# Optimization experiments

Hardware: AMD Instinct MI355X
Metric: run time of the kernel (lower is better)

The kernel has to match this reference:

```python
import jax, jax.numpy as jnp
import numpy as np

IN_DIM = 64
OUT_DIM = 64
ATTN_DIM = 5
N_REL = 200
N_ENT = 40000
N_NODE = 500000
N_EDGE = 1000000
BATCH = 32


def setup_inputs() -> dict:
    key = jax.random.key(0)
    ks = jax.random.split(key, 20)
    n_rel_emb = 2 * N_REL + 1
    # forward args
    q_sub = jax.random.randint(ks[0], (BATCH,), 0, N_ENT)
    q_rel = jax.random.randint(ks[1], (BATCH,), 0, n_rel_emb)
    hidden = jax.random.normal(ks[2], (N_NODE, IN_DIM), dtype=jnp.float32)
    # edges columns: 0=batch idx, 1=unused, 2=rel, 3=unused, 4=sub, 5=obj
    e_batch = jax.random.randint(ks[3], (N_EDGE,), 0, BATCH)
    e_rel = jax.random.randint(ks[4], (N_EDGE,), 0, n_rel_emb)
    e_sub = jax.random.randint(ks[5], (N_EDGE,), 0, N_NODE)
    e_obj = jax.random.randint(ks[6], (N_EDGE,), 0, N_NODE)
    edges = jnp.stack([e_batch, e_batch, e_rel, e_rel, e_sub, e_obj], axis=1)
    nodes = jnp.stack([jax.random.randint(ks[7], (N_NODE,), 0, BATCH),
                       jax.random.randint(ks[8], (N_NODE,), 0, N_ENT)], axis=1)
    old_nodes_new_idx = jax.random.randint(ks[9], (100000,), 0, N_NODE)
    # parameters (stored as [in, out]; torch Linear does x @ W.T + b)
    def lin(k, fan_in, fan_out):
        b = 1.0 / np.sqrt(fan_in)
        return jax.random.uniform(k, (fan_in, fan_out), jnp.float32, -b, b)
    rela_embed = jax.random.normal(ks[10], (n_rel_emb, IN_DIM), dtype=jnp.float32)
    return {
        "hidden": hidden,
        "rela_embed": rela_embed,
        "Ws": lin(ks[11], IN_DIM, ATTN_DIM),
        "Wr": lin(ks[12], IN_DIM, ATTN_DIM),
        "Wqr_w": lin(ks[13], IN_DIM, ATTN_DIM),
        "Wqr_b": jnp.zeros((ATTN_DIM,), jnp.float32),
        "walpha_w": lin(ks[14], ATTN_DIM, 1),
        "walpha_b": jnp.zeros((1,), jnp.float32),
        "Wh": lin(ks[15], IN_DIM, OUT_DIM),
        "attn_fc_w": lin(ks[16], 2 * OUT_DIM, 1),
        "attn_fc_b": jnp.zeros((1,), jnp.float32),
        "Wnode_w": lin(ks[17], OUT_DIM, OUT_DIM),
        "Wnode_b": jnp.zeros((OUT_DIM,), jnp.float32),
        "q_sub": q_sub,
        "q_rel": q_rel,
        "edges": edges,
        "nodes": nodes,
        "old_nodes_new_idx": old_nodes_new_idx,
        "batchsize": BATCH,
    }


def reference(hidden, rela_embed, Ws, Wr, Wqr_w, Wqr_b, walpha_w, walpha_b,
              Wh, attn_fc_w, attn_fc_b, Wnode_w, Wnode_b,
              q_sub, q_rel, edges, nodes, old_nodes_new_idx, batchsize):
    n_node = nodes.shape[0]
    r_idx, rel, sub, obj = edges[:, 0], edges[:, 2], edges[:, 4], edges[:, 5]
    hs = hidden[sub]                      # [E, in_dim] gather
    hr = rela_embed[rel]                  # [E, in_dim]
    h_qr = rela_embed[q_rel][r_idx]       # [E, in_dim]
    message = hs - hr                     # [E, in_dim]
    attn = jax.nn.relu(hs @ Ws + hr @ Wr + h_qr @ Wqr_w + Wqr_b)   # [E, attn_dim]
    alpha = jax.nn.sigmoid(attn @ walpha_w + walpha_b)             # [E, 1]
    message = alpha * message
    # scatter-max over obj; empty segments filled with 0 (torch_scatter semantics)
    agg = jax.ops.segment_max(message, obj, num_segments=n_node)   # [n_node, in_dim]
    agg = jnp.where(jnp.isneginf(agg), 0.0, agg)
    hidden_new = agg @ Wh                 # act = identity        [n_node, out_dim]
    # edge attention over new node states
    cat = jnp.concatenate([hidden_new[sub], hidden_new[obj]], axis=-1)  # [E, 2*out]
    scores = jax.nn.leaky_relu((cat @ attn_fc_w + attn_fc_b)[:, 0], 0.2)  # [E]
    # source code overwrites scatter_softmax with a global softmax over all edges
    w = jax.nn.softmax(scores)            # [E]
    msg2 = w[:, None] * (hidden_new[obj] @ Wnode_w + Wnode_b)      # [E, out_dim]
    hidden_new = jax.ops.segment_sum(msg2, sub, num_segments=n_node)
    return hidden_new
```

## Files before the change

### kernel.cpp

```cpp
#include <hip/hip_runtime.h>
#include <math.h>
#include <float.h>


#define SCAN_BLK 256
#define SCAN_ITEMS 4
#define SCAN_CHUNK (SCAN_BLK * SCAN_ITEMS)
#define SOFT_G 2048
#define NPW 8

__global__ void k_tables(const float* __restrict__ rela, const float* __restrict__ Wr,
                         const float* __restrict__ Wqr_w, const float* __restrict__ Wqr_b,
                         const int* __restrict__ q_rel,
                         float* __restrict__ s2, float* __restrict__ s3,
                         int nrel, int batch) {
  int tid = blockIdx.x * blockDim.x + threadIdx.x;
  int stride = gridDim.x * blockDim.x;
  for (int idx = tid; idx < nrel * 5; idx += stride) {
    int r = idx / 5, j = idx % 5;
    float acc = 0.f;
    for (int k = 0; k < 64; k++) acc += rela[r * 64 + k] * Wr[k * 5 + j];
    s2[idx] = acc;
  }
  for (int idx = tid; idx < batch * 5; idx += stride) {
    int b = idx / 5, j = idx % 5;
    int qr = q_rel[b];
    float acc = Wqr_b[j];
    for (int k = 0; k < 64; k++) acc += rela[qr * 64 + k] * Wqr_w[k * 5 + j];
    s3[idx] = acc;
  }
}

__global__ void k_fuse(const float* __restrict__ Wh, const float* __restrict__ Wn,
                       const float* __restrict__ fw,
                       float* __restrict__ W2, float* __restrict__ fuv) {
  int tid = threadIdx.x;
  for (int idx = tid; idx < 64 * 64; idx += 256) {
    int k = idx >> 6, m = idx & 63;
    float acc = 0.f;
    for (int j = 0; j < 64; j++) acc += Wh[k * 64 + j] * Wn[j * 64 + m];
    W2[idx] = acc;
  }
  if (tid < 128) {
    int k = tid & 63, h = tid >> 6;
    float acc = 0.f;
    for (int j = 0; j < 64; j++) acc += Wh[k * 64 + j] * fw[h * 64 + j];
    fuv[h * 64 + k] = acc;
  }
}

__global__ void __launch_bounds__(256, 2)
k_proj(const float* __restrict__ hidden, const float* __restrict__ Ws_g,
       float* __restrict__ P, int N) {
  int n = blockIdx.x * blockDim.x + threadIdx.x;
  if (n >= N) return;
  float hs[64];
  const float4* h4 = (const float4*)(hidden + (size_t)n * 64);
#pragma unroll
  for (int k4 = 0; k4 < 16; k4++) {
    float4 h = h4[k4];
    hs[k4 * 4 + 0] = h.x; hs[k4 * 4 + 1] = h.y; hs[k4 * 4 + 2] = h.z; hs[k4 * 4 + 3] = h.w;
  }
  float acc[5] = {0.f, 0.f, 0.f, 0.f, 0.f};
#pragma unroll
  for (int k = 0; k < 64; k++) {
    float h = hs[k];
#pragma unroll
    for (int j = 0; j < 5; j++) acc[j] += h * Ws_g[k * 5 + j];
  }
#pragma unroll
  for (int j = 0; j < 5; j++) P[(size_t)n * 5 + j] = acc[j];
}

__global__ void k_hist(const int* __restrict__ edges, int* __restrict__ cnt, int E, int N) {
  int e = blockIdx.x * blockDim.x + threadIdx.x;
  if (e < E) {
    int sub = edges[e * 6 + 4];
    int obj = edges[e * 6 + 5];
    atomicAdd(&cnt[obj], 1);
    atomicAdd(&cnt[N + sub], 1);
  }
}

__global__ void k_scan_partial(const int* __restrict__ cnt, int* __restrict__ part, int n) {
  __shared__ int sdata[SCAN_BLK];
  int base = blockIdx.x * SCAN_CHUNK + threadIdx.x * SCAN_ITEMS;
  int s = 0;
#pragma unroll
  for (int j = 0; j < SCAN_ITEMS; j++) { int i = base + j; if (i < n) s += cnt[i]; }
  sdata[threadIdx.x] = s;
  __syncthreads();
  for (int d = SCAN_BLK / 2; d > 0; d >>= 1) {
    if (threadIdx.x < d) sdata[threadIdx.x] += sdata[threadIdx.x + d];
    __syncthreads();
  }
  if (threadIdx.x == 0) part[blockIdx.x] = sdata[0];
}

__global__ void k_scan_top(int* part, int nblk) {
  __shared__ int lds[1024];
  int tid = threadIdx.x;
  int v = (tid < nblk) ? part[tid] : 0;
  lds[tid] = v;
  __syncthreads();
  for (int d = 1; d < 1024; d <<= 1) {
    int t = (tid >= d) ? lds[tid - d] : 0;
    __syncthreads();
    lds[tid] += t;
    __syncthreads();
  }
  if (tid < nblk) part[tid] = lds[tid] - v;
}

__global__ void k_scan_final(const int* __restrict__ cnt, const int* __restrict__ part,
                             int* __restrict__ off, int n) {
  __shared__ int lds[SCAN_BLK];
  int tid = threadIdx.x;
  int base = blockIdx.x * SCAN_CHUNK + tid * SCAN_ITEMS;
  int c[SCAN_ITEMS];
  int s = 0;
#pragma unroll
  for (int j = 0; j < SCAN_ITEMS; j++) { int i = base + j; c[j] = (i < n) ? cnt[i] : 0; s += c[j]; }
  int v = s;
  lds[tid] = s;
  __syncthreads();
  for (int d = 1; d < SCAN_BLK; d <<= 1) {
    int t = (tid >= d) ? lds[tid - d] : 0;
    __syncthreads();
    lds[tid] += t;
    __syncthreads();
  }
  int run = part[blockIdx.x] + (lds[tid] - v);
#pragma unroll
  for (int j = 0; j < SCAN_ITEMS; j++) { int i = base + j; if (i < n) off[i] = run; run += c[j]; }
}

__global__ void k_scatter(const int* __restrict__ edges, const float* __restrict__ P,
                          const float* __restrict__ s2, const float* __restrict__ s3,
                          const float* __restrict__ walpha_w, const float* __restrict__ walpha_b,
                          int* __restrict__ cur, int4* __restrict__ rec_obj,
                          int2* __restrict__ rec_sub, int E, int N) {
  int e = blockIdx.x * blockDim.x + threadIdx.x;
  if (e >= E) return;
  int ridx = edges[e * 6 + 0];
  int rel  = edges[e * 6 + 2];
  int sub  = edges[e * 6 + 4];
  int obj  = edges[e * 6 + 5];
  float z = walpha_b[0];
#pragma unroll
  for (int j = 0; j < 5; j++) {
    float vj = P[(size_t)sub * 5 + j] + s2[rel * 5 + j] + s3[ridx * 5 + j];
    z += fmaxf(vj, 0.f) * walpha_w[j];
  }
  float a = 1.f / (1.f + expf(-z));
  int p = atomicAdd(&cur[obj], 1);
  rec_obj[p] = make_int4(sub, rel, __float_as_int(a), 0);
  int q = atomicAdd(&cur[N + sub], 1) - E;
  rec_sub[q] = make_int2(obj, sub);
}

__global__ void k_agg(const int* __restrict__ off, const int4* __restrict__ rec_obj,
                      const float* __restrict__ hidden, const float* __restrict__ rela,
                      float* __restrict__ agg, int N) {
  int lane = threadIdx.x & 63;
  int wid  = blockIdx.x * (blockDim.x >> 6) + (threadIdx.x >> 6);
  int node0 = wid * NPW;
  if (node0 >= N) return;
  int ov = 0;
  if (lane <= NPW) {
    int idx = node0 + lane;
    if (idx > N) idx = N;
    ov = off[idx];
  }
  int B   = __shfl(ov, 0);
  int End = __shfl(ov, NPW);
  int lbase = B;
  int rx = 0, ry = 0; float rz = 0.f;
  {
    int p = lbase + lane;
    if (p < End) { int4 r = rec_obj[p]; rx = r.x; ry = r.y; rz = __int_as_float(r.z); }
  }
  int cur = B;
  for (int i = 0; i < NPW; i++) {
    int node = node0 + i;
    if (node >= N) break;
    int en = __shfl(ov, i + 1);
    int bst = cur;
    float vmax = -FLT_MAX;
    while (cur < en) {
      int idx = cur - lbase;
      if (idx >= 64) {
        lbase += 64;
        int p = lbase + lane;
        if (p < End) { int4 r = rec_obj[p]; rx = r.x; ry = r.y; rz = __int_as_float(r.z); }
        idx = 0;
      }
      int sub = __shfl(rx, idx);
      int rel = __shfl(ry, idx);
      float a = __shfl(rz, idx);
      float x = a * (hidden[(size_t)sub * 64 + lane] - rela[rel * 64 + lane]);
      vmax = fmaxf(vmax, x);
      cur++;
    }
    agg[(size_t)node * 64 + lane] = (en > bst) ? vmax : 0.f;
  }
}

__global__ void __launch_bounds__(128)
k_trans(float* A, const float* __restrict__ W2, const float* __restrict__ fuv,
        float* __restrict__ u, float* __restrict__ v, int N) {
  __shared__ float lds[64 * 64];
  int tid = threadIdx.x;
  int n0 = blockIdx.x * 128;
  int n = n0 + tid;
  bool act = (n < N);
  float acc[64];
  if (act) {
    float a[64];
    const float4* A4 = (const float4*)(A + (size_t)n * 64);
#pragma unroll
    for (int q = 0; q < 16; q++) {
      float4 h = A4[q];
      a[q * 4 + 0] = h.x; a[q * 4 + 1] = h.y; a[q * 4 + 2] = h.z; a[q * 4 + 3] = h.w;
    }
    float uacc = 0.f, vacc = 0.f;
#pragma unroll
    for (int k = 0; k < 64; k++) {
      uacc += a[k] * fuv[k];
      vacc += a[k] * fuv[64 + k];
    }
    u[n] = uacc;
    v[n] = vacc;
#pragma unroll
    for (int j = 0; j < 64; j++) acc[j] = 0.f;
#pragma unroll
    for (int k = 0; k < 64; k++) {
      float ak = a[k];
#pragma unroll
      for (int j = 0; j < 64; j++) acc[j] += ak * W2[k * 64 + j];
    }
  }
  for (int ph = 0; ph < 2; ph++) {
    if (act && (tid >> 6) == ph) {
      int r = tid & 63;
#pragma unroll
      for (int g = 0; g < 16; g++) {
        int pos = g ^ (tid & 15);
        *(float4*)&lds[r * 64 + pos * 4] =
            make_float4(acc[g * 4], acc[g * 4 + 1], acc[g * 4 + 2], acc[g * 4 + 3]);
      }
    }
    __syncthreads();
    float4* Cg = (float4*)(A + (size_t)(n0 + ph * 64) * 64);
#pragma unroll
    for (int i = 0; i < 8; i++) {
      int f = tid + 128 * i;
      int row = f >> 4, c4 = f & 15;
      if (n0 + ph * 64 + row < N) {
        int pos = c4 ^ (row & 15);
        Cg[f] = *(float4*)&lds[row * 64 + pos * 4];
      }
    }
    __syncthreads();
  }
}

__global__ void k_scores(const int2* __restrict__ rec_sub, const float* __restrict__ u,
                         const float* __restrict__ v, const float* __restrict__ fb,
                         float* __restrict__ scores, float* __restrict__ pmax,
                         float* __restrict__ psum, int E) {
  __shared__ float red_m[256], red_s[256];
  float b = fb[0];
  float lm = -FLT_MAX, ls = 0.f;
  for (int pos = blockIdx.x * blockDim.x + threadIdx.x; pos < E; pos += gridDim.x * blockDim.x) {
    int2 r = rec_sub[pos];
    float s = u[r.y] + v[r.x] + b;
    s = (s >= 0.f) ? s : 0.2f * s;
    scores[pos] = s;
    if (s > lm) { ls = ls * expf(lm - s) + 1.f; lm = s; }
    else        { ls += expf(s - lm); }
  }
  red_m[threadIdx.x] = lm; red_s[threadIdx.x] = ls;
  __syncthreads();
  for (int d = blockDim.x / 2; d > 0; d >>= 1) {
    if (threadIdx.x < d) {
      float m1 = red_m[threadIdx.x], s1 = red_s[threadIdx.x];
      float m2 = red_m[threadIdx.x + d], s2 = red_s[threadIdx.x + d];
      float m = fmaxf(m1, m2);
      float s = 0.f;
      if (m > -FLT_MAX) s = s1 * expf(m1 - m) + s2 * expf(m2 - m);
      red_m[threadIdx.x] = m; red_s[threadIdx.x] = s;
    }
    __syncthreads();
  }
  if (threadIdx.x == 0) { pmax[blockIdx.x] = red_m[0]; psum[blockIdx.x] = red_s[0]; }
}

__global__ void k_softmax_final(const float* __restrict__ pmax, const float* __restrict__ psum,
                                float* __restrict__ scal, int G) {
  __shared__ float red_m[256], red_s[256];
  float lm = -FLT_MAX, ls = 0.f;
  for (int i = threadIdx.x; i < G; i += 256) {
    float m2 = pmax[i], s2 = psum[i];
    if (m2 > lm) { ls = ls * expf(lm - m2) + s2; lm = m2; }
    else         { ls += s2 * expf(m2 - lm); }
  }
  red_m[threadIdx.x] = lm; red_s[threadIdx.x] = ls;
  __syncthreads();
  for (int d = 128; d > 0; d >>= 1) {
    if (threadIdx.x < d) {
      float m1 = red_m[threadIdx.x], s1 = red_s[threadIdx.x];
      float m2 = red_m[threadIdx.x + d], s2 = red_s[threadIdx.x + d];
      float m = fmaxf(m1, m2);
      float s = 0.f;
      if (m > -FLT_MAX) s = s1 * expf(m1 - m) + s2 * expf(m2 - m);
      red_m[threadIdx.x] = m; red_s[threadIdx.x] = s;
    }
    __syncthreads();
  }
  if (threadIdx.x == 0) { scal[0] = red_m[0]; scal[1] = red_s[0]; }
}

__global__ void k_expw(float* __restrict__ scores, const float* __restrict__ scal, int E) {
  int i = blockIdx.x * blockDim.x + threadIdx.x;
  if (i < E) scores[i] = expf(scores[i] - scal[0]);
}

__global__ void k_aggsum(const int* __restrict__ off, const int2* __restrict__ rec_sub,
                         const float* __restrict__ wexp, const float* __restrict__ agg2,
                         const float* __restrict__ bias, const float* __restrict__ scal,
                         float* __restrict__ out, int N, int E) {
  int lane = threadIdx.x & 63;
  int wid  = blockIdx.x * (blockDim.x >> 6) + (threadIdx.x >> 6);
  int node0 = wid * NPW;
  if (node0 >= N) return;
  float bl = bias[lane];
  float inv = 1.f / scal[1];
  int ov = 0;
  if (lane <= NPW) {
    int idx = node0 + lane;
    ov = (idx >= N) ? E : (off[N + idx] - E);
  }
  int B   = __shfl(ov, 0);
  int End = __shfl(ov, NPW);
  int lbase = B;
  int objr = 0; float wr = 0.f;
  {
    int p = lbase + lane;
    if (p < End) { objr = rec_sub[p].x; wr = wexp[p]; }
  }
  int cur = B;
  for (int i = 0; i < NPW; i++) {
    int node = node0 + i;
    if (node >= N) break;
    int en = __shfl(ov, i + 1);
    float acc = 0.f, wa = 0.f;
    while (cur < en) {
      int idx = cur - lbase;
      if (idx >= 64) {
        lbase += 64;
        int p = lbase + lane;
        if (p < End) { objr = rec_sub[p].x; wr = wexp[p]; }
        idx = 0;
      }
      int obj = __shfl(objr, idx);
      float ww = __shfl(wr, idx);
      acc += ww * agg2[(size_t)obj * 64 + lane];
      wa  += ww;
      cur++;
    }
    out[(size_t)node * 64 + lane] = (acc + wa * bl) * inv;
  }
}

extern "C" void kernel_launch(void* const* d_in, const int* in_sizes, int n_in,
                              void* d_out, int out_size, void* d_ws, size_t ws_size,
                              hipStream_t stream) {
  const float* hidden    = (const float*)d_in[0];
  const float* rela      = (const float*)d_in[1];
  const float* Ws        = (const float*)d_in[2];
  const float* Wr        = (const float*)d_in[3];
  const float* Wqr_w     = (const float*)d_in[4];
  const float* Wqr_b     = (const float*)d_in[5];
  const float* walpha_w  = (const float*)d_in[6];
  const float* walpha_b  = (const float*)d_in[7];
  const float* Wh        = (const float*)d_in[8];
  const float* attn_fc_w = (const float*)d_in[9];
  const float* attn_fc_b = (const float*)d_in[10];
  const float* Wnode_w   = (const float*)d_in[11];
  const float* Wnode_b   = (const float*)d_in[12];
  const int*   q_rel     = (const int*)d_in[14];
  const int*   edges     = (const int*)d_in[15];

  int N = in_sizes[0] / 64;
  int E = in_sizes[15] / 6;
  int nrel = in_sizes[1] / 64;
  int batch = in_sizes[14];

  char* w = (char*)d_ws;
  size_t o = 0;
  #define WS_ALLOC(ptr_t, name, bytes) \
    ptr_t name = (ptr_t)(w + o); o = (o + (size_t)(bytes) + 255) & ~(size_t)255;
  WS_ALLOC(float*, aggT,    (size_t)N * 64 * 4)
  WS_ALLOC(float*, P,       (size_t)N * 5 * 4)
  WS_ALLOC(int4*,  rec_obj, (size_t)E * 16)
  WS_ALLOC(int2*,  rec_sub, (size_t)E * 8)
  WS_ALLOC(int*,   cnt,     (size_t)2 * N * 4)
  WS_ALLOC(int*,   off,     (size_t)2 * N * 4)
  WS_ALLOC(int*,   part,    1024 * 4)
  WS_ALLOC(float*, pmax,    SOFT_G * 4)
  WS_ALLOC(float*, psum,    SOFT_G * 4)
  WS_ALLOC(float*, s2t,     (size_t)nrel * 5 * 4)
  WS_ALLOC(float*, s3t,     (size_t)batch * 5 * 4)
  WS_ALLOC(float*, scal,    2 * 4)
  WS_ALLOC(float*, W2,      64 * 64 * 4)
  WS_ALLOC(float*, fuv,     2 * 64 * 4)
  #undef WS_ALLOC

  float* u = P;
  float* v = P + N;
  float* scores = (float*)cnt;

  k_tables<<<16, 256, 0, stream>>>(rela, Wr, Wqr_w, Wqr_b, q_rel, s2t, s3t, nrel, batch);
  k_fuse<<<1, 256, 0, stream>>>(Wh, Wnode_w, attn_fc_w, W2, fuv);
  k_proj<<<(N + 255) / 256, 256, 0, stream>>>(hidden, Ws, P, N);
  hipMemsetAsync(cnt, 0, (size_t)2 * N * 4, stream);
  k_hist<<<(E + 255) / 256, 256, 0, stream>>>(edges, cnt, E, N);
  int SCAN_N = 2 * N;
  int nblk = (SCAN_N + SCAN_CHUNK - 1) / SCAN_CHUNK;
  k_scan_partial<<<nblk, SCAN_BLK, 0, stream>>>(cnt, part, SCAN_N);
  k_scan_top<<<1, 1024, 0, stream>>>(part, nblk);
  k_scan_final<<<nblk, SCAN_BLK, 0, stream>>>(cnt, part, off, SCAN_N);
  hipMemcpyAsync(cnt, off, (size_t)2 * N * 4, hipMemcpyDeviceToDevice, stream);
  k_scatter<<<(E + 255) / 256, 256, 0, stream>>>(edges, P, s2t, s3t, walpha_w, walpha_b,
                                                 cnt, rec_obj, rec_sub, E, N);
  int csr_blocks = (N + NPW * 4 - 1) / (NPW * 4);
  k_agg<<<csr_blocks, 256, 0, stream>>>(off, rec_obj, hidden, rela, aggT, N);
  k_trans<<<(N + 127) / 128, 128, 0, stream>>>(aggT, W2, fuv, u, v, N);
  k_scores<<<SOFT_G, 256, 0, stream>>>(rec_sub, u, v, attn_fc_b, scores, pmax, psum, E);
  k_softmax_final<<<1, 256, 0, stream>>>(pmax, psum, scal, SOFT_G);
  k_expw<<<(E + 255) / 256, 256, 0, stream>>>(scores, scal, E);
  k_aggsum<<<csr_blocks, 256, 0, stream>>>(off, rec_sub, scores , aggT ,
                                           Wnode_b, scal, (float*)d_out, N, E);
}
```

Baseline: 784.8 us.

## Fuse node transform and attention projections into the scatter-max aggregation kernel

Merges the separate per-node 64x64 transform kernel into the CSR max-aggregation kernel. Each wavefront keeps one column of the fused weight matrix in registers, stages its aggregated rows in shared memory, computes u/v with wave shuffle reductions, and writes the transformed rows directly. This removes one full write and read of the N x 64 intermediate and one kernel launch. In exchange it adds 64 weight registers per lane plus shared memory in the aggregation kernel, which may lower occupancy for this latency-bound gather.

```diff
diff --git a/kernel.cpp b/kernel.cpp
--- a/kernel.cpp
+++ b/kernel.cpp
@@ -159,13 +159,21 @@
   rec_sub[q] = make_int2(obj, sub);
 }
 
-__global__ void k_agg(const int* __restrict__ off, const int4* __restrict__ rec_obj,
-                      const float* __restrict__ hidden, const float* __restrict__ rela,
-                      float* __restrict__ agg, int N) {
-  int lane = threadIdx.x & 63;
-  int wid  = blockIdx.x * (blockDim.x >> 6) + (threadIdx.x >> 6);
+__global__ void k_agg2(const int* __restrict__ off, const int4* __restrict__ rec_obj,
+                       const float* __restrict__ hidden, const float* __restrict__ rela,
+                       const float* __restrict__ W2, const float* __restrict__ fuv,
+                       float* __restrict__ agg2, float* __restrict__ u, float* __restrict__ v,
+                       int N) {
+  __shared__ float rows[4][NPW][64];
+  int lane  = threadIdx.x & 63;
+  int wslot = threadIdx.x >> 6;
+  int wid   = blockIdx.x * (blockDim.x >> 6) + wslot;
   int node0 = wid * NPW;
   if (node0 >= N) return;
+  float wl[64];
+#pragma unroll
+  for (int k = 0; k < 64; k++) wl[k] = W2[k * 64 + lane];
+  float fu = fuv[lane], fv = fuv[64 + lane];
   int ov = 0;
   if (lane <= NPW) {
     int idx = node0 + lane;
@@ -202,66 +210,30 @@
       vmax = fmaxf(vmax, x);
       cur++;
     }
-    agg[(size_t)node * 64 + lane] = (en > bst) ? vmax : 0.f;
-  }
-}
-
-__global__ void __launch_bounds__(128)
-k_trans(float* A, const float* __restrict__ W2, const float* __restrict__ fuv,
-        float* __restrict__ u, float* __restrict__ v, int N) {
-  __shared__ float lds[64 * 64];
-  int tid = threadIdx.x;
-  int n0 = blockIdx.x * 128;
-  int n = n0 + tid;
-  bool act = (n < N);
-  float acc[64];
-  if (act) {
-    float a[64];
-    const float4* A4 = (const float4*)(A + (size_t)n * 64);
-#pragma unroll
-    for (int q = 0; q < 16; q++) {
-      float4 h = A4[q];
-      a[q * 4 + 0] = h.x; a[q * 4 + 1] = h.y; a[q * 4 + 2] = h.z; a[q * 4 + 3] = h.w;
-    }
-    float uacc = 0.f, vacc = 0.f;
-#pragma unroll
-    for (int k = 0; k < 64; k++) {
-      uacc += a[k] * fuv[k];
-      vacc += a[k] * fuv[64 + k];
-    }
-    u[n] = uacc;
-    v[n] = vacc;
-#pragma unroll
-    for (int j = 0; j < 64; j++) acc[j] = 0.f;
-#pragma unroll
-    for (int k = 0; k < 64; k++) {
-      float ak = a[k];
-#pragma unroll
-      for (int j = 0; j < 64; j++) acc[j] += ak * W2[k * 64 + j];
-    }
-  }
-  for (int ph = 0; ph < 2; ph++) {
-    if (act && (tid >> 6) == ph) {
-      int r = tid & 63;
-#pragma unroll
-      for (int g = 0; g < 16; g++) {
-        int pos = g ^ (tid & 15);
-        *(float4*)&lds[r * 64 + pos * 4] =
-            make_float4(acc[g * 4], acc[g * 4 + 1], acc[g * 4 + 2], acc[g * 4 + 3]);
-      }
-    }
-    __syncthreads();
-    float4* Cg = (float4*)(A + (size_t)(n0 + ph * 64) * 64);
-#pragma unroll
-    for (int i = 0; i < 8; i++) {
-      int f = tid + 128 * i;
-      int row = f >> 4, c4 = f & 15;
-      if (n0 + ph * 64 + row < N) {
-        int pos = c4 ^ (row & 15);
-        Cg[f] = *(float4*)&lds[row * 64 + pos * 4];
-      }
-    }
-    __syncthreads();
+    float rowv = (en > bst) ? vmax : 0.f;
+    rows[wslot][i][lane] = rowv;
+    float ur = rowv * fu, vr = rowv * fv;
+#pragma unroll
+    for (int m = 32; m > 0; m >>= 1) {
+      ur += __shfl_xor(ur, m);
+      vr += __shfl_xor(vr, m);
+    }
+    if (lane == 0) { u[node] = ur; v[node] = vr; }
+  }
+  for (int i = 0; i < NPW; i++) {
+    int node = node0 + i;
+    if (node >= N) break;
+    const float4* rp = (const float4*)rows[wslot][i];
+    float acc = 0.f;
+#pragma unroll
+    for (int k4 = 0; k4 < 16; k4++) {
+      float4 r4 = rp[k4];
+      acc = fmaf(r4.x, wl[k4 * 4 + 0], acc);
+      acc = fmaf(r4.y, wl[k4 * 4 + 1], acc);
+      acc = fmaf(r4.z, wl[k4 * 4 + 2], acc);
+      acc = fmaf(r4.w, wl[k4 * 4 + 3], acc);
+    }
+    agg2[(size_t)node * 64 + lane] = acc;
   }
 }
 
@@ -401,7 +373,7 @@
   size_t o = 0;
   #define WS_ALLOC(ptr_t, name, bytes) \
     ptr_t name = (ptr_t)(w + o); o = (o + (size_t)(bytes) + 255) & ~(size_t)255;
-  WS_ALLOC(float*, aggT,    (size_t)N * 64 * 4)
+  WS_ALLOC(float*, agg2,    (size_t)N * 64 * 4)
   WS_ALLOC(float*, P,       (size_t)N * 5 * 4)
   WS_ALLOC(int4*,  rec_obj, (size_t)E * 16)
   WS_ALLOC(int2*,  rec_sub, (size_t)E * 8)
@@ -435,11 +407,11 @@
   k_scatter<<<(E + 255) / 256, 256, 0, stream>>>(edges, P, s2t, s3t, walpha_w, walpha_b,
                                                  cnt, rec_obj, rec_sub, E, N);
   int csr_blocks = (N + NPW * 4 - 1) / (NPW * 4);
-  k_agg<<<csr_blocks, 256, 0, stream>>>(off, rec_obj, hidden, rela, aggT, N);
-  k_trans<<<(N + 127) / 128, 128, 0, stream>>>(aggT, W2, fuv, u, v, N);
+  k_agg2<<<csr_blocks, 256, 0, stream>>>(off, rec_obj, hidden, rela, W2, fuv,
+                                         agg2, u, v, N);
   k_scores<<<SOFT_G, 256, 0, stream>>>(rec_sub, u, v, attn_fc_b, scores, pmax, psum, E);
   k_softmax_final<<<1, 256, 0, stream>>>(pmax, psum, scal, SOFT_G);
   k_expw<<<(E + 255) / 256, 256, 0, stream>>>(scores, scal, E);
-  k_aggsum<<<csr_blocks, 256, 0, stream>>>(off, rec_sub, scores , aggT ,
+  k_aggsum<<<csr_blocks, 256, 0, stream>>>(off, rec_sub, scores , agg2,
                                            Wnode_b, scal, (float*)d_out, N, E);
 }
```

After: 829.4 us. 1.06x slower.

## Fuse prep, histogram and projection kernels; split transform by column halves

Applied to the files above, without the earlier changes.

Merges the two table kernels and the counter memset into one prep kernel, fuses node projection into the edge histogram kernel, and has the scan write the cursor copy directly instead of a device memcpy. The softmax exponent is folded into the final aggregation, removing a separate pass over the edge scores. The dense transform is split across two column halves via a 2D grid: aggregates go to the output buffer, results go to a separate buffer, and each thread keeps 32 accumulators instead of 64. This cuts launches and register pressure, at the cost of reading the aggregate rows twice and computing exp per lane during aggregation.

```diff
diff --git a/kernel.cpp b/kernel.cpp
--- a/kernel.cpp
+++ b/kernel.cpp
@@ -9,13 +9,17 @@
 #define SOFT_G 2048
 #define NPW 8
 
-__global__ void k_tables(const float* __restrict__ rela, const float* __restrict__ Wr,
-                         const float* __restrict__ Wqr_w, const float* __restrict__ Wqr_b,
-                         const int* __restrict__ q_rel,
-                         float* __restrict__ s2, float* __restrict__ s3,
-                         int nrel, int batch) {
+__global__ void k_prep(const float* __restrict__ rela, const float* __restrict__ Wr,
+                       const float* __restrict__ Wqr_w, const float* __restrict__ Wqr_b,
+                       const int* __restrict__ q_rel, const float* __restrict__ Wh,
+                       const float* __restrict__ Wn, const float* __restrict__ fw,
+                       float* __restrict__ s2, float* __restrict__ s3,
+                       float* __restrict__ W2, float* __restrict__ fuv,
+                       int* __restrict__ cnt,
+                       int nrel, int batch, int n2) {
   int tid = blockIdx.x * blockDim.x + threadIdx.x;
   int stride = gridDim.x * blockDim.x;
+  for (int i = tid; i < n2; i += stride) cnt[i] = 0;
   for (int idx = tid; idx < nrel * 5; idx += stride) {
     int r = idx / 5, j = idx % 5;
     float acc = 0.f;
@@ -29,56 +33,47 @@
     for (int k = 0; k < 64; k++) acc += rela[qr * 64 + k] * Wqr_w[k * 5 + j];
     s3[idx] = acc;
   }
-}
-
-__global__ void k_fuse(const float* __restrict__ Wh, const float* __restrict__ Wn,
-                       const float* __restrict__ fw,
-                       float* __restrict__ W2, float* __restrict__ fuv) {
-  int tid = threadIdx.x;
-  for (int idx = tid; idx < 64 * 64; idx += 256) {
+  for (int idx = tid; idx < 64 * 64; idx += stride) {
     int k = idx >> 6, m = idx & 63;
     float acc = 0.f;
     for (int j = 0; j < 64; j++) acc += Wh[k * 64 + j] * Wn[j * 64 + m];
     W2[idx] = acc;
   }
-  if (tid < 128) {
-    int k = tid & 63, h = tid >> 6;
+  for (int idx = tid; idx < 128; idx += stride) {
+    int k = idx & 63, h = idx >> 6;
     float acc = 0.f;
     for (int j = 0; j < 64; j++) acc += Wh[k * 64 + j] * fw[h * 64 + j];
     fuv[h * 64 + k] = acc;
   }
 }
 
-__global__ void __launch_bounds__(256, 2)
-k_proj(const float* __restrict__ hidden, const float* __restrict__ Ws_g,
-       float* __restrict__ P, int N) {
-  int n = blockIdx.x * blockDim.x + threadIdx.x;
-  if (n >= N) return;
-  float hs[64];
-  const float4* h4 = (const float4*)(hidden + (size_t)n * 64);
-#pragma unroll
-  for (int k4 = 0; k4 < 16; k4++) {
-    float4 h = h4[k4];
-    hs[k4 * 4 + 0] = h.x; hs[k4 * 4 + 1] = h.y; hs[k4 * 4 + 2] = h.z; hs[k4 * 4 + 3] = h.w;
-  }
-  float acc[5] = {0.f, 0.f, 0.f, 0.f, 0.f};
-#pragma unroll
-  for (int k = 0; k < 64; k++) {
-    float h = hs[k];
-#pragma unroll
-    for (int j = 0; j < 5; j++) acc[j] += h * Ws_g[k * 5 + j];
-  }
-#pragma unroll
-  for (int j = 0; j < 5; j++) P[(size_t)n * 5 + j] = acc[j];
-}
-
-__global__ void k_hist(const int* __restrict__ edges, int* __restrict__ cnt, int E, int N) {
-  int e = blockIdx.x * blockDim.x + threadIdx.x;
-  if (e < E) {
-    int sub = edges[e * 6 + 4];
-    int obj = edges[e * 6 + 5];
+__global__ void k_proj_hist(const float* __restrict__ hidden, const float* __restrict__ Ws_g,
+                            const int* __restrict__ edges, float* __restrict__ P,
+                            int* __restrict__ cnt, int N, int E) {
+  int g = blockIdx.x * blockDim.x + threadIdx.x;
+  if (g < E) {
+    int sub = edges[g * 6 + 4];
+    int obj = edges[g * 6 + 5];
     atomicAdd(&cnt[obj], 1);
     atomicAdd(&cnt[N + sub], 1);
+  }
+  if (g < N) {
+    float hs[64];
+    const float4* h4 = (const float4*)(hidden + (size_t)g * 64);
+#pragma unroll
+    for (int k4 = 0; k4 < 16; k4++) {
+      float4 h = h4[k4];
+      hs[k4 * 4 + 0] = h.x; hs[k4 * 4 + 1] = h.y; hs[k4 * 4 + 2] = h.z; hs[k4 * 4 + 3] = h.w;
+    }
+    float acc[5] = {0.f, 0.f, 0.f, 0.f, 0.f};
+#pragma unroll
+    for (int k = 0; k < 64; k++) {
+      float h = hs[k];
+#pragma unroll
+      for (int j = 0; j < 5; j++) acc[j] += h * Ws_g[k * 5 + j];
+    }
+#pragma unroll
+    for (int j = 0; j < 5; j++) P[(size_t)g * 5 + j] = acc[j];
   }
 }
 
@@ -112,7 +107,7 @@
   if (tid < nblk) part[tid] = lds[tid] - v;
 }
 
-__global__ void k_scan_final(const int* __restrict__ cnt, const int* __restrict__ part,
+__global__ void k_scan_final(int* __restrict__ cnt, const int* __restrict__ part,
                              int* __restrict__ off, int n) {
   __shared__ int lds[SCAN_BLK];
   int tid = threadIdx.x;
@@ -132,7 +127,11 @@
   }
   int run = part[blockIdx.x] + (lds[tid] - v);
 #pragma unroll
-  for (int j = 0; j < SCAN_ITEMS; j++) { int i = base + j; if (i < n) off[i] = run; run += c[j]; }
+  for (int j = 0; j < SCAN_ITEMS; j++) {
+    int i = base + j;
+    if (i < n) { off[i] = run; cnt[i] = run; }
+    run += c[j];
+  }
 }
 
 __global__ void k_scatter(const int* __restrict__ edges, const float* __restrict__ P,
@@ -197,7 +196,7 @@
       }
       int sub = __shfl(rx, idx);
       int rel = __shfl(ry, idx);
-      float a = __shfl(rz, idx);
+      float a = __int_as_float(__shfl(__float_as_int(rz), idx));
       float x = a * (hidden[(size_t)sub * 64 + lane] - rela[rel * 64 + lane]);
       vmax = fmaxf(vmax, x);
       cur++;
@@ -207,61 +206,53 @@
 }
 
 __global__ void __launch_bounds__(128)
-k_trans(float* A, const float* __restrict__ W2, const float* __restrict__ fuv,
-        float* __restrict__ u, float* __restrict__ v, int N) {
-  __shared__ float lds[64 * 64];
+k_trans2(const float* __restrict__ A, const float* __restrict__ W2,
+         const float* __restrict__ fuv, float* __restrict__ Bo,
+         float* __restrict__ u, float* __restrict__ v, int N) {
+  __shared__ float lds[128 * 32];
   int tid = threadIdx.x;
+  int h = blockIdx.y;
   int n0 = blockIdx.x * 128;
   int n = n0 + tid;
-  bool act = (n < N);
-  float acc[64];
-  if (act) {
-    float a[64];
+  if (n < N) {
+    float acc[32];
+#pragma unroll
+    for (int j = 0; j < 32; j++) acc[j] = 0.f;
+    float uvacc = 0.f;
+    const float* fvec = fuv + h * 64;
+    const float* Wb = W2 + h * 32;
     const float4* A4 = (const float4*)(A + (size_t)n * 64);
 #pragma unroll
-    for (int q = 0; q < 16; q++) {
-      float4 h = A4[q];
-      a[q * 4 + 0] = h.x; a[q * 4 + 1] = h.y; a[q * 4 + 2] = h.z; a[q * 4 + 3] = h.w;
-    }
-    float uacc = 0.f, vacc = 0.f;
-#pragma unroll
-    for (int k = 0; k < 64; k++) {
-      uacc += a[k] * fuv[k];
-      vacc += a[k] * fuv[64 + k];
-    }
-    u[n] = uacc;
-    v[n] = vacc;
-#pragma unroll
-    for (int j = 0; j < 64; j++) acc[j] = 0.f;
-#pragma unroll
-    for (int k = 0; k < 64; k++) {
-      float ak = a[k];
-#pragma unroll
-      for (int j = 0; j < 64; j++) acc[j] += ak * W2[k * 64 + j];
-    }
-  }
-  for (int ph = 0; ph < 2; ph++) {
-    if (act && (tid >> 6) == ph) {
-      int r = tid & 63;
-#pragma unroll
-      for (int g = 0; g < 16; g++) {
-        int pos = g ^ (tid & 15);
-        *(float4*)&lds[r * 64 + pos * 4] =
-            make_float4(acc[g * 4], acc[g * 4 + 1], acc[g * 4 + 2], acc[g * 4 + 3]);
+    for (int k4 = 0; k4 < 16; k4++) {
+      float4 a4 = A4[k4];
+      float av[4] = {a4.x, a4.y, a4.z, a4.w};
+#pragma unroll
+      for (int q = 0; q < 4; q++) {
+        int k = k4 * 4 + q;
+        float ak = av[q];
+        uvacc += ak * fvec[k];
+#pragma unroll
+        for (int j = 0; j < 32; j++) acc[j] += ak * Wb[k * 64 + j];
       }
     }
-    __syncthreads();
-    float4* Cg = (float4*)(A + (size_t)(n0 + ph * 64) * 64);
-#pragma unroll
-    for (int i = 0; i < 8; i++) {
-      int f = tid + 128 * i;
-      int row = f >> 4, c4 = f & 15;
-      if (n0 + ph * 64 + row < N) {
-        int pos = c4 ^ (row & 15);
-        Cg[f] = *(float4*)&lds[row * 64 + pos * 4];
-      }
-    }
-    __syncthreads();
+    if (h == 0) u[n] = uvacc; else v[n] = uvacc;
+#pragma unroll
+    for (int j4 = 0; j4 < 8; j4++) {
+      int pos = j4 ^ (tid & 7);
+      *(float4*)&lds[tid * 32 + pos * 4] =
+          make_float4(acc[j4 * 4], acc[j4 * 4 + 1], acc[j4 * 4 + 2], acc[j4 * 4 + 3]);
+    }
+  }
+  __syncthreads();
+#pragma unroll
+  for (int i = 0; i < 8; i++) {
+    int f = tid + 128 * i;
+    int row = f >> 3, c4 = f & 7;
+    if (n0 + row < N) {
+      int pos = c4 ^ (row & 7);
+      *(float4*)&Bo[(size_t)(n0 + row) * 64 + h * 32 + c4 * 4] =
+          *(float4*)&lds[row * 32 + pos * 4];
+    }
   }
 }
 
@@ -321,13 +312,8 @@
   if (threadIdx.x == 0) { scal[0] = red_m[0]; scal[1] = red_s[0]; }
 }
 
-__global__ void k_expw(float* __restrict__ scores, const float* __restrict__ scal, int E) {
-  int i = blockIdx.x * blockDim.x + threadIdx.x;
-  if (i < E) scores[i] = expf(scores[i] - scal[0]);
-}
-
 __global__ void k_aggsum(const int* __restrict__ off, const int2* __restrict__ rec_sub,
-                         const float* __restrict__ wexp, const float* __restrict__ agg2,
+                         const float* __restrict__ scores, const float* __restrict__ agg2,
                          const float* __restrict__ bias, const float* __restrict__ scal,
                          float* __restrict__ out, int N, int E) {
   int lane = threadIdx.x & 63;
@@ -335,6 +321,7 @@
   int node0 = wid * NPW;
   if (node0 >= N) return;
   float bl = bias[lane];
+  float gmax = scal[0];
   float inv = 1.f / scal[1];
   int ov = 0;
   if (lane <= NPW) {
@@ -347,7 +334,7 @@
   int objr = 0; float wr = 0.f;
   {
     int p = lbase + lane;
-    if (p < End) { objr = rec_sub[p].x; wr = wexp[p]; }
+    if (p < End) { objr = rec_sub[p].x; wr = expf(scores[p] - gmax); }
   }
   int cur = B;
   for (int i = 0; i < NPW; i++) {
@@ -360,11 +347,11 @@
       if (idx >= 64) {
         lbase += 64;
         int p = lbase + lane;
-        if (p < End) { objr = rec_sub[p].x; wr = wexp[p]; }
+        if (p < End) { objr = rec_sub[p].x; wr = expf(scores[p] - gmax); }
         idx = 0;
       }
       int obj = __shfl(objr, idx);
-      float ww = __shfl(wr, idx);
+      float ww = __int_as_float(__shfl(__float_as_int(wr), idx));
       acc += ww * agg2[(size_t)obj * 64 + lane];
       wa  += ww;
       cur++;
@@ -401,7 +388,7 @@
   size_t o = 0;
   #define WS_ALLOC(ptr_t, name, bytes) \
     ptr_t name = (ptr_t)(w + o); o = (o + (size_t)(bytes) + 255) & ~(size_t)255;
-  WS_ALLOC(float*, aggT,    (size_t)N * 64 * 4)
+  WS_ALLOC(float*, agg2,    (size_t)N * 64 * 4)
   WS_ALLOC(float*, P,       (size_t)N * 5 * 4)
   WS_ALLOC(int4*,  rec_obj, (size_t)E * 16)
   WS_ALLOC(int2*,  rec_sub, (size_t)E * 8)
@@ -420,26 +407,24 @@
   float* u = P;
   float* v = P + N;
   float* scores = (float*)cnt;
-
-  k_tables<<<16, 256, 0, stream>>>(rela, Wr, Wqr_w, Wqr_b, q_rel, s2t, s3t, nrel, batch);
-  k_fuse<<<1, 256, 0, stream>>>(Wh, Wnode_w, attn_fc_w, W2, fuv);
-  k_proj<<<(N + 255) / 256, 256, 0, stream>>>(hidden, Ws, P, N);
-  hipMemsetAsync(cnt, 0, (size_t)2 * N * 4, stream);
-  k_hist<<<(E + 255) / 256, 256, 0, stream>>>(edges, cnt, E, N);
+  float* aggbuf = (float*)d_out;
+
+  k_prep<<<256, 256, 0, stream>>>(rela, Wr, Wqr_w, Wqr_b, q_rel, Wh, Wnode_w, attn_fc_w,
+                                  s2t, s3t, W2, fuv, cnt, nrel, batch, 2 * N);
+  k_proj_hist<<<(E + 255) / 256, 256, 0, stream>>>(hidden, Ws, edges, P, cnt, N, E);
   int SCAN_N = 2 * N;
   int nblk = (SCAN_N + SCAN_CHUNK - 1) / SCAN_CHUNK;
   k_scan_partial<<<nblk, SCAN_BLK, 0, stream>>>(cnt, part, SCAN_N);
   k_scan_top<<<1, 1024, 0, stream>>>(part, nblk);
   k_scan_final<<<nblk, SCAN_BLK, 0, stream>>>(cnt, part, off, SCAN_N);
-  hipMemcpyAsync(cnt, off, (size_t)2 * N * 4, hipMemcpyDeviceToDevice, stream);
   k_scatter<<<(E + 255) / 256, 256, 0, stream>>>(edges, P, s2t, s3t, walpha_w, walpha_b,
                                                  cnt, rec_obj, rec_sub, E, N);
   int csr_blocks = (N + NPW * 4 - 1) / (NPW * 4);
-  k_agg<<<csr_blocks, 256, 0, stream>>>(off, rec_obj, hidden, rela, aggT, N);
-  k_trans<<<(N + 127) / 128, 128, 0, stream>>>(aggT, W2, fuv, u, v, N);
+  k_agg<<<csr_blocks, 256, 0, stream>>>(off, rec_obj, hidden, rela, aggbuf, N);
+  dim3 tgrid((N + 127) / 128, 2);
+  k_trans2<<<tgrid, 128, 0, stream>>>(aggbuf, W2, fuv, agg2, u, v, N);
   k_scores<<<SOFT_G, 256, 0, stream>>>(rec_sub, u, v, attn_fc_b, scores, pmax, psum, E);
   k_softmax_final<<<1, 256, 0, stream>>>(pmax, psum, scal, SOFT_G);
-  k_expw<<<(E + 255) / 256, 256, 0, stream>>>(scores, scal, E);
-  k_aggsum<<<csr_blocks, 256, 0, stream>>>(off, rec_sub, scores , aggT ,
+  k_aggsum<<<csr_blocks, 256, 0, stream>>>(off, rec_sub, scores, agg2,
                                            Wnode_b, scal, (float*)d_out, N, E);
 }
```

Measured after the change: 730.4 us. -6.9%, faster.
